# Performance work log

Measured on AMD Instinct MI355X. Metric: run time of the kernel, lower is better.

Reference implementation:

```python
import jax, jax.numpy as jnp
import numpy as np

STRIDE = 2
PAD = 1
K = 4
OUT_PAD = 0


def setup_inputs() -> dict:
    key = jax.random.key(0)
    k1, k2, k3, k4 = jax.random.split(key, 4)
    x = jax.random.normal(k1, (16, 64, 128, 128), dtype=jnp.float32)
    # torch ConvTranspose2d weight layout: [in_channels, out_channels, kH, kW]
    w = jax.random.normal(k2, (64, 32, 4, 4), dtype=jnp.float32) * 0.05
    conv_b = jax.random.normal(k3, (32,), dtype=jnp.float32) * 0.05
    bias = jax.random.normal(k4, (1, 1, 1, 1), dtype=jnp.float32)
    return {"x": x, "w": w, "conv_b": conv_b, "bias": bias}


def conv_transpose2d(x, w, conv_b):
    # Equivalent of torch ConvTranspose2d(k=4, s=2, p=1, op=0):
    # dilate input by stride, pad by k-1-p (+op on trailing side), conv with flipped kernel.
    lo = K - 1 - PAD
    hi = K - 1 - PAD + OUT_PAD
    w_oihw = jnp.flip(w, axis=(2, 3)).transpose(1, 0, 2, 3)  # [Cout, Cin, kH, kW]
    y = jax.lax.conv_general_dilated(
        x, w_oihw,
        window_strides=(1, 1),
        padding=((lo, hi), (lo, hi)),
        lhs_dilation=(STRIDE, STRIDE),
        dimension_numbers=("NCHW", "OIHW", "NCHW"),
    )
    return y + conv_b[None, :, None, None]


def reference(x, w, conv_b, bias):
    y = conv_transpose2d(x, w, conv_b)          # [N, Cout, H', W']
    y = jnp.min(y, axis=1, keepdims=True)       # channel-min -> [N,1,H',W']
    y = jnp.sum(y, axis=2, keepdims=True)       # height-sum  -> [N,1,1,W']
    # kernel uses tanh-based GELU approximation
    return jax.nn.gelu(y, approximate=True) + bias
```

## Files before the change

kernel.cpp:

```cpp
#include <hip/hip_runtime.h>
#include <math.h>

typedef __attribute__((ext_vector_type(8))) short short8;
typedef __attribute__((ext_vector_type(16))) float f32x16;
typedef __attribute__((ext_vector_type(2))) unsigned uintx2;

#define XS_STRIDE 72
#define RING 6

__device__ __forceinline__ short f2bf(float f) {
    union { float f; unsigned u; } v; v.f = f;
    unsigned r = (v.u + 0x7FFFu + ((v.u >> 16) & 1u)) >> 16;
    return (short)r;
}

__device__ __forceinline__ unsigned cvt_pk_bf16(float lo, float hi) {
    unsigned r;
    asm("v_cvt_pk_bf16_f32 %0, %1, %2" : "=v"(r) : "v"(lo), "v"(hi));
    return r;
}

__device__ __forceinline__ void bar_nodrain() {
    __builtin_amdgcn_sched_barrier(0);
    asm volatile("s_waitcnt lgkmcnt(0)" ::: "memory");
    __builtin_amdgcn_s_barrier();
    __builtin_amdgcn_sched_barrier(0);
}

__global__ void prep(const float* __restrict__ w, short* __restrict__ wfrag) {
    int idx = blockIdx.x * 256 + threadIdx.x;
    int j    = idx & 7;
    int lane = (idx >> 3) & 63;
    int q    = (idx >> 9) & 15;
    int p    = idx >> 13;
    int co = lane & 31, hf = lane >> 5;
    int ci = (q & 3) * 16 + hf * 8 + j;
    int tq = q >> 2, a = tq >> 1, b = tq & 1;
    int ph = p >> 1, pw = p & 1;
    int kh = 2 * a + 1 - ph, kw = 2 * b + 1 - pw;
    wfrag[idx] = f2bf(w[((ci * 32 + co) * 4 + kh) * 4 + kw]);
}

__global__ __launch_bounds__(256, 3) void convt_mfma(
    const float* __restrict__ x, const short* __restrict__ wfrag,
    const float* __restrict__ conv_b, float* __restrict__ partials)
{
    __shared__ short xs[RING][34][XS_STRIDE];
    __shared__ float minbuf[2][2][4][32];

    int blk = ((blockIdx.x & 7) << 7) | (blockIdx.x >> 3);
    const int jq = blk & 3;
    const int st = (blk >> 2) & 15;
    const int n  = blk >> 6;
    const int t  = threadIdx.x;
    const int i0 = st * 8;

    const int wv = t >> 6, lane = t & 63;
    const int ph = wv >> 1, pw = wv & 1;
    const int ln = lane & 31, half = lane >> 5;

    short8 af[16];
    {
        const short8* wf = (const short8*)(wfrag + wv * 8192);
        #pragma unroll
        for (int q = 0; q < 16; ++q) af[q] = wf[q * 64 + lane];
    }
    float cb[16];
    #pragma unroll
    for (int reg = 0; reg < 16; ++reg)
        cb[reg] = conv_b[(reg & 3) + 8 * (reg >> 2) + 4 * half];

    const float* xn = x + (size_t)n * 64 * 128 * 128;

    const int col  = t & 31;
    const int cib  = (t >> 5) * 8;
    const int gcol = jq * 32 + col;
    const int hrow = t >> 7, hside = (t >> 6) & 1, hci = t & 63;
    const int hgc  = jq * 32 + (hside ? 32 : -1);
    const int sl_base = i0 % RING;

    #pragma unroll
    for (int r = 0; r < 4; ++r) {
        int gi = i0 - 1 + r;
        int slot = sl_base + r; if (slot >= RING) slot -= RING;
        bool rowok = (unsigned)gi < 128u;
        int gic = rowok ? gi : 0;
        const float* px = xn + ((size_t)cib * 128 + gic) * 128 + gcol;
        float v[8];
        #pragma unroll
        for (int c = 0; c < 8; ++c) v[c] = rowok ? px[c * 16384] : 0.f;
        uintx2 u0, u1;
        u0.x = cvt_pk_bf16(v[0], v[1]); u0.y = cvt_pk_bf16(v[2], v[3]);
        u1.x = cvt_pk_bf16(v[4], v[5]); u1.y = cvt_pk_bf16(v[6], v[7]);
        *(uintx2*)&xs[slot][col + 1][cib]     = u0;
        *(uintx2*)&xs[slot][col + 1][cib + 4] = u1;
    }
    {
        int r = t >> 6, ci = t & 63, gi = i0 - 1 + r;
        int slot = sl_base + r; if (slot >= RING) slot -= RING;
        #pragma unroll
        for (int side = 0; side < 2; ++side) {
            int gc = jq * 32 + (side ? 32 : -1);
            float v = ((unsigned)gi < 128u && (unsigned)gc < 128u)
                    ? xn[((size_t)ci * 128 + gi) * 128 + gc] : 0.f;
            xs[slot][side ? 33 : 0][ci] = f2bf(v);
        }
    }

    float pf[2][8]; float pfh;
    auto issue = [&](int r0) {
        #pragma unroll
        for (int r2 = 0; r2 < 2; ++r2) {
            int gi = r0 + r2;
            bool rowok = (unsigned)gi < 128u;
            int gic = rowok ? gi : 0;
            const float* px = xn + ((size_t)cib * 128 + gic) * 128 + gcol;
            #pragma unroll
            for (int c = 0; c < 8; ++c) pf[r2][c] = rowok ? px[c * 16384] : 0.f;
        }
        int gi = r0 + hrow;
        pfh = ((unsigned)gi < 128u && (unsigned)hgc < 128u)
            ? xn[((size_t)hci * 128 + gi) * 128 + hgc] : 0.f;
    };
    issue(i0 + 3);

    bar_nodrain();

    float osum = 0.f;
    const int rpr = t >> 6;
    const int pw2 = (t >> 5) & 1;
    const int jl  = t & 31;

    int rbase = sl_base;
    #pragma unroll
    for (int k = 0; k < 4; ++k) {
        const int kb = k & 1;
        int s0 = rbase + ph; if (s0 >= RING) s0 -= RING;
        int s1 = s0 + 1;     if (s1 >= RING) s1 -= RING;
        int s2 = s1 + 1;     if (s2 >= RING) s2 -= RING;

        f32x16 acc0, acc1;
        #pragma unroll
        for (int reg = 0; reg < 16; ++reg) { acc0[reg] = cb[reg]; acc1[reg] = cb[reg]; }
        __builtin_amdgcn_s_setprio(1);
        #pragma unroll
        for (int b = 0; b < 2; ++b) {
            int colp = ln + (pw - b) + 1;
            const short* p0 = &xs[s0][colp][half * 8];
            const short* p1 = &xs[s1][colp][half * 8];
            const short* p2 = &xs[s2][colp][half * 8];
            #pragma unroll
            for (int c = 0; c < 4; ++c) {
                short8 Fs = *(const short8*)(p1 + c * 16);
                acc0 = __builtin_amdgcn_mfma_f32_32x32x16_bf16(af[4*b+c],   Fs, acc0, 0, 0, 0);
                acc1 = __builtin_amdgcn_mfma_f32_32x32x16_bf16(af[8+4*b+c], Fs, acc1, 0, 0, 0);
                short8 F0 = *(const short8*)(p0 + c * 16);
                acc0 = __builtin_amdgcn_mfma_f32_32x32x16_bf16(af[8+4*b+c], F0, acc0, 0, 0, 0);
                short8 F2 = *(const short8*)(p2 + c * 16);
                acc1 = __builtin_amdgcn_mfma_f32_32x32x16_bf16(af[4*b+c],   F2, acc1, 0, 0, 0);
            }
        }
        __builtin_amdgcn_s_setprio(0);

        float mn0, mn1;
        {
            float a = fminf(fminf(acc0[0], acc0[1]), fminf(acc0[2], acc0[3]));
            float b2 = fminf(fminf(acc0[4], acc0[5]), fminf(acc0[6], acc0[7]));
            float c = fminf(fminf(acc0[8], acc0[9]), fminf(acc0[10], acc0[11]));
            float d = fminf(fminf(acc0[12], acc0[13]), fminf(acc0[14], acc0[15]));
            mn0 = fminf(fminf(a, b2), fminf(c, d));
            a = fminf(fminf(acc1[0], acc1[1]), fminf(acc1[2], acc1[3]));
            b2 = fminf(fminf(acc1[4], acc1[5]), fminf(acc1[6], acc1[7]));
            c = fminf(fminf(acc1[8], acc1[9]), fminf(acc1[10], acc1[11]));
            d = fminf(fminf(acc1[12], acc1[13]), fminf(acc1[14], acc1[15]));
            mn1 = fminf(fminf(a, b2), fminf(c, d));
        }
        mn0 = fminf(mn0, __shfl_xor(mn0, 32, 64));
        mn1 = fminf(mn1, __shfl_xor(mn1, 32, 64));
        if (half == 0) {
            minbuf[kb][0][wv][ln] = mn0;
            minbuf[kb][1][wv][ln] = mn1;
        }

        if (k < 3) {
            int ws0 = rbase + 4; if (ws0 >= RING) ws0 -= RING;
            int ws1 = ws0 + 1;   if (ws1 >= RING) ws1 -= RING;
            #pragma unroll
            for (int r2 = 0; r2 < 2; ++r2) {
                int slot = r2 ? ws1 : ws0;
                uintx2 u0, u1;
                u0.x = cvt_pk_bf16(pf[r2][0], pf[r2][1]);
                u0.y = cvt_pk_bf16(pf[r2][2], pf[r2][3]);
                u1.x = cvt_pk_bf16(pf[r2][4], pf[r2][5]);
                u1.y = cvt_pk_bf16(pf[r2][6], pf[r2][7]);
                *(uintx2*)&xs[slot][col + 1][cib]     = u0;
                *(uintx2*)&xs[slot][col + 1][cib + 4] = u1;
            }
            xs[hrow ? ws1 : ws0][hside ? 33 : 0][hci] = f2bf(pfh);
            if (k < 2) issue(i0 + 2 * k + 5);
        }
        bar_nodrain();
        if (t < 128)
            osum += minbuf[kb][rpr][pw2][jl] + minbuf[kb][rpr][2 + pw2][jl];
        rbase += 2; if (rbase >= RING) rbase -= RING;
    }

    float* sbuf = &minbuf[0][0][0][0];
    if (t < 128) sbuf[t] = osum;
    bar_nodrain();
    if (t < 64) {
        float v = sbuf[t] + sbuf[t + 64];
        int ow = ((jq * 32 + (t & 31)) << 1) | ((t >> 5) & 1);
        partials[(size_t)st * 4096 + n * 256 + ow] = v;
    }
}

__global__ void finalize(const float* __restrict__ partials,
                         const float* __restrict__ bias, float* __restrict__ out)
{
    int idx = blockIdx.x * 256 + threadIdx.x;
    float s = 0.f;
    #pragma unroll
    for (int st = 0; st < 16; ++st) s += partials[st * 4096 + idx];
    float u = 0.7978845608028654f * (s + 0.044715f * s * s * s);
    out[idx] = 0.5f * s * (1.f + tanhf(u)) + bias[0];
}

extern "C" void kernel_launch(void* const* d_in, const int* in_sizes, int n_in,
                              void* d_out, int out_size, void* d_ws, size_t ws_size,
                              hipStream_t stream) {
    const float* x      = (const float*)d_in[0];
    const float* w      = (const float*)d_in[1];
    const float* conv_b = (const float*)d_in[2];
    const float* bias   = (const float*)d_in[3];
    float* out = (float*)d_out;

    short* wfrag    = (short*)d_ws;
    float* partials = (float*)((char*)d_ws + 65536);

    hipLaunchKernelGGL(prep, dim3(128), dim3(256), 0, stream, w, wfrag);
    hipLaunchKernelGGL(convt_mfma, dim3(16 * 16 * 4), dim3(256), 0, stream,
                       x, wfrag, conv_b, partials);
    hipLaunchKernelGGL(finalize, dim3(16), dim3(256), 0, stream,
                       partials, bias, out);
}
```

Measured before the change: 129.4 us.

## Replace ring-buffered row prefetch with full upfront LDS staging

The 6-slot LDS ring, refilled between compute steps, is replaced by a 10-row LDS tile (with halo columns) that is loaded completely before any MFMA work starts. The per-step barriers and the per-step minbuf exchange go away: each wave keeps its running sum of channel-minimums in a register, and a single LDS reduction runs at the end. This removes in-loop synchronisation and ring index arithmetic. In exchange, a block can no longer overlap its own loads with compute, so latency hiding depends on the other resident blocks, and LDS per block grows to about 49 KB, which may affect occupancy.

```diff
diff --git a/kernel.cpp b/kernel.cpp
--- a/kernel.cpp
+++ b/kernel.cpp
@@ -6,7 +6,7 @@
 typedef __attribute__((ext_vector_type(2))) unsigned uintx2;
 
 #define XS_STRIDE 72
-#define RING 6
+#define NROWS 10
 
 __device__ __forceinline__ short f2bf(float f) {
     union { float f; unsigned u; } v; v.f = f;
@@ -20,11 +20,9 @@
     return r;
 }
 
-__device__ __forceinline__ void bar_nodrain() {
-    __builtin_amdgcn_sched_barrier(0);
+__device__ __forceinline__ void bar_lds() {
     asm volatile("s_waitcnt lgkmcnt(0)" ::: "memory");
     __builtin_amdgcn_s_barrier();
-    __builtin_amdgcn_sched_barrier(0);
 }
 
 __global__ void prep(const float* __restrict__ w, short* __restrict__ wfrag) {
@@ -45,8 +43,8 @@
     const float* __restrict__ x, const short* __restrict__ wfrag,
     const float* __restrict__ conv_b, float* __restrict__ partials)
 {
-    __shared__ short xs[RING][34][XS_STRIDE];
-    __shared__ float minbuf[2][2][4][32];
+    __shared__ short xs[NROWS][34][XS_STRIDE];
+    __shared__ float minbuf[4][32];
 
     int blk = ((blockIdx.x & 7) << 7) | (blockIdx.x >> 3);
     const int jq = blk & 3;
@@ -75,70 +73,56 @@
     const int col  = t & 31;
     const int cib  = (t >> 5) * 8;
     const int gcol = jq * 32 + col;
-    const int hrow = t >> 7, hside = (t >> 6) & 1, hci = t & 63;
-    const int hgc  = jq * 32 + (hside ? 32 : -1);
-    const int sl_base = i0 % RING;
-
-    #pragma unroll
-    for (int r = 0; r < 4; ++r) {
+
+    float hv[5];
+    #pragma unroll
+    for (int q = 0; q < 5; ++q) {
+        int idx = q * 256 + t;
+        int r = idx >> 7, side = (idx >> 6) & 1, ci = idx & 63;
         int gi = i0 - 1 + r;
-        int slot = sl_base + r; if (slot >= RING) slot -= RING;
+        int gc = jq * 32 + (side ? 32 : -1);
+        hv[q] = ((unsigned)gi < 128u && (unsigned)gc < 128u)
+              ? xn[((size_t)ci * 128 + gi) * 128 + gc] : 0.f;
+    }
+
+    float pfA[8], pfB[8];
+    auto load_row = [&](int r, float* dst) {
+        int gi = i0 - 1 + r;
         bool rowok = (unsigned)gi < 128u;
         int gic = rowok ? gi : 0;
         const float* px = xn + ((size_t)cib * 128 + gic) * 128 + gcol;
-        float v[8];
-        #pragma unroll
-        for (int c = 0; c < 8; ++c) v[c] = rowok ? px[c * 16384] : 0.f;
+        #pragma unroll
+        for (int c = 0; c < 8; ++c) dst[c] = rowok ? px[c * 16384] : 0.f;
+    };
+    auto write_row = [&](int r, const float* src) {
         uintx2 u0, u1;
-        u0.x = cvt_pk_bf16(v[0], v[1]); u0.y = cvt_pk_bf16(v[2], v[3]);
-        u1.x = cvt_pk_bf16(v[4], v[5]); u1.y = cvt_pk_bf16(v[6], v[7]);
-        *(uintx2*)&xs[slot][col + 1][cib]     = u0;
-        *(uintx2*)&xs[slot][col + 1][cib + 4] = u1;
-    }
-    {
-        int r = t >> 6, ci = t & 63, gi = i0 - 1 + r;
-        int slot = sl_base + r; if (slot >= RING) slot -= RING;
-        #pragma unroll
-        for (int side = 0; side < 2; ++side) {
-            int gc = jq * 32 + (side ? 32 : -1);
-            float v = ((unsigned)gi < 128u && (unsigned)gc < 128u)
-                    ? xn[((size_t)ci * 128 + gi) * 128 + gc] : 0.f;
-            xs[slot][side ? 33 : 0][ci] = f2bf(v);
-        }
-    }
-
-    float pf[2][8]; float pfh;
-    auto issue = [&](int r0) {
-        #pragma unroll
-        for (int r2 = 0; r2 < 2; ++r2) {
-            int gi = r0 + r2;
-            bool rowok = (unsigned)gi < 128u;
-            int gic = rowok ? gi : 0;
-            const float* px = xn + ((size_t)cib * 128 + gic) * 128 + gcol;
-            #pragma unroll
-            for (int c = 0; c < 8; ++c) pf[r2][c] = rowok ? px[c * 16384] : 0.f;
-        }
-        int gi = r0 + hrow;
-        pfh = ((unsigned)gi < 128u && (unsigned)hgc < 128u)
-            ? xn[((size_t)hci * 128 + gi) * 128 + hgc] : 0.f;
+        u0.x = cvt_pk_bf16(src[0], src[1]); u0.y = cvt_pk_bf16(src[2], src[3]);
+        u1.x = cvt_pk_bf16(src[4], src[5]); u1.y = cvt_pk_bf16(src[6], src[7]);
+        *(uintx2*)&xs[r][col + 1][cib]     = u0;
+        *(uintx2*)&xs[r][col + 1][cib + 4] = u1;
     };
-    issue(i0 + 3);
-
-    bar_nodrain();
+    load_row(0, pfA);
+    load_row(1, pfB);
+    #pragma unroll
+    for (int r = 0; r < NROWS; r += 2) {
+        write_row(r, pfA);
+        if (r + 2 < NROWS) load_row(r + 2, pfA);
+        write_row(r + 1, pfB);
+        if (r + 3 < NROWS) load_row(r + 3, pfB);
+    }
+    #pragma unroll
+    for (int q = 0; q < 5; ++q) {
+        int idx = q * 256 + t;
+        int r = idx >> 7, side = (idx >> 6) & 1, ci = idx & 63;
+        xs[r][side ? 33 : 0][ci] = f2bf(hv[q]);
+    }
+
+    bar_lds();
 
     float osum = 0.f;
-    const int rpr = t >> 6;
-    const int pw2 = (t >> 5) & 1;
-    const int jl  = t & 31;
-
-    int rbase = sl_base;
     #pragma unroll
     for (int k = 0; k < 4; ++k) {
-        const int kb = k & 1;
-        int s0 = rbase + ph; if (s0 >= RING) s0 -= RING;
-        int s1 = s0 + 1;     if (s1 >= RING) s1 -= RING;
-        int s2 = s1 + 1;     if (s2 >= RING) s2 -= RING;
-
+        const int L0 = 2 * k + ph;
         f32x16 acc0, acc1;
         #pragma unroll
         for (int reg = 0; reg < 16; ++reg) { acc0[reg] = cb[reg]; acc1[reg] = cb[reg]; }
@@ -146,9 +130,9 @@
         #pragma unroll
         for (int b = 0; b < 2; ++b) {
             int colp = ln + (pw - b) + 1;
-            const short* p0 = &xs[s0][colp][half * 8];
-            const short* p1 = &xs[s1][colp][half * 8];
-            const short* p2 = &xs[s2][colp][half * 8];
+            const short* p0 = &xs[L0][colp][half * 8];
+            const short* p1 = &xs[L0 + 1][colp][half * 8];
+            const short* p2 = &xs[L0 + 2][colp][half * 8];
             #pragma unroll
             for (int c = 0; c < 4; ++c) {
                 short8 Fs = *(const short8*)(p1 + c * 16);
@@ -177,40 +161,16 @@
         }
         mn0 = fminf(mn0, __shfl_xor(mn0, 32, 64));
         mn1 = fminf(mn1, __shfl_xor(mn1, 32, 64));
-        if (half == 0) {
-            minbuf[kb][0][wv][ln] = mn0;
-            minbuf[kb][1][wv][ln] = mn1;
-        }
-
-        if (k < 3) {
-            int ws0 = rbase + 4; if (ws0 >= RING) ws0 -= RING;
-            int ws1 = ws0 + 1;   if (ws1 >= RING) ws1 -= RING;
-            #pragma unroll
-            for (int r2 = 0; r2 < 2; ++r2) {
-                int slot = r2 ? ws1 : ws0;
-                uintx2 u0, u1;
-                u0.x = cvt_pk_bf16(pf[r2][0], pf[r2][1]);
-                u0.y = cvt_pk_bf16(pf[r2][2], pf[r2][3]);
-                u1.x = cvt_pk_bf16(pf[r2][4], pf[r2][5]);
-                u1.y = cvt_pk_bf16(pf[r2][6], pf[r2][7]);
-                *(uintx2*)&xs[slot][col + 1][cib]     = u0;
-                *(uintx2*)&xs[slot][col + 1][cib + 4] = u1;
-            }
-            xs[hrow ? ws1 : ws0][hside ? 33 : 0][hci] = f2bf(pfh);
-            if (k < 2) issue(i0 + 2 * k + 5);
-        }
-        bar_nodrain();
-        if (t < 128)
-            osum += minbuf[kb][rpr][pw2][jl] + minbuf[kb][rpr][2 + pw2][jl];
-        rbase += 2; if (rbase >= RING) rbase -= RING;
-    }
-
-    float* sbuf = &minbuf[0][0][0][0];
-    if (t < 128) sbuf[t] = osum;
-    bar_nodrain();
+        osum += mn0 + mn1;
+    }
+
+    if (half == 0) minbuf[wv][ln] = osum;
+    bar_lds();
+
     if (t < 64) {
-        float v = sbuf[t] + sbuf[t + 64];
-        int ow = ((jq * 32 + (t & 31)) << 1) | ((t >> 5) & 1);
+        int c = t & 31, pwp = t >> 5;
+        float v = minbuf[pwp][c] + minbuf[2 + pwp][c];
+        int ow = ((jq * 32 + c) << 1) | pwp;
         partials[(size_t)st * 4096 + n * 256 + ow] = v;
     }
 }
```

Result: faster. 115.8 us (-10.5%).
